# Optimization experiments

Measured on AMD Instinct MI355X. Metric: run time of the kernel, lower is better.

Reference implementation:

```python
import jax, jax.numpy as jnp
import numpy as np

B, L, H, V, G, TGB = 128, 512, 256, 100000, 4, 128
S = 2 * L - 1  # max_sequence_tokens = 2*history_capacity - 1


def setup_inputs() -> dict:
    key = jax.random.key(0)
    ks = jax.random.split(key, 16)
    d = {}
    d['history_tokens'] = jax.random.randint(ks[0], (B, L), 0, V)
    d['history_post_tokens'] = jax.random.randint(ks[1], (B, L), 0, V)
    d['history_author_tokens'] = jax.random.randint(ks[2], (B, L), 0, V)
    d['history_action_tokens'] = jax.random.randint(ks[3], (B, L), 0, V)
    d['history_time_gap'] = jax.random.randint(ks[4], (B, L), 0, TGB + 1)
    d['history_group_ids'] = jnp.sort(jax.random.randint(ks[5], (B, L), 0, G + 1), axis=-1)
    d['lengths'] = jax.random.randint(ks[6], (B,), 0, L + 1)
    # embedding tables (padding_idx=0 rows zeroed as in nn.Embedding(padding_idx=0))
    d['token_table'] = (jax.random.normal(ks[7], (V, H)) * 0.02).at[0].set(0.0)
    d['time_table'] = (jax.random.normal(ks[8], (TGB + 1, H)) * 0.02).at[0].set(0.0)
    d['group_table'] = (jax.random.normal(ks[9], (G + 1, H)) * 0.02).at[0].set(0.0)
    d['pos_table'] = jax.random.normal(ks[10], (S, H)) * 0.02
    d['sep_token'] = jax.random.normal(ks[11], (H,)) * 0.02
    # event_projection params: LayerNorm(6H) -> Linear(6H,4H) -> SiLU -> Linear(4H,H)
    d['ln_gamma'] = jnp.ones((6 * H,), jnp.float32)
    d['ln_beta'] = jnp.zeros((6 * H,), jnp.float32)
    d['W1'] = jax.random.normal(ks[12], (6 * H, 4 * H)) * (1.0 / np.sqrt(6 * H))
    d['b1'] = jnp.zeros((4 * H,), jnp.float32)
    d['W2'] = jax.random.normal(ks[13], (4 * H, H)) * (1.0 / np.sqrt(4 * H))
    d['b2'] = jnp.zeros((H,), jnp.float32)
    return d


def _layernorm(x, g, b, eps=1e-5):
    m = x.mean(-1, keepdims=True)
    v = x.var(-1, keepdims=True)
    return (x - m) / jnp.sqrt(v + eps) * g + b


def reference(history_tokens, history_post_tokens, history_author_tokens,
              history_action_tokens, history_time_gap, history_group_ids,
              lengths, token_table, time_table, group_table, pos_table,
              sep_token, ln_gamma, ln_beta, W1, b1, W2, b2):
    # --- event embedding: 6 lookups concat -> LN -> MLP  (dropout is eval no-op)
    ev = jnp.concatenate([
        token_table[history_tokens],
        token_table[history_post_tokens],
        token_table[history_author_tokens],
        token_table[history_action_tokens],
        time_table[jnp.clip(history_time_gap, 0, TGB)],
        group_table[history_group_ids],
    ], axis=-1)  # [B, L, 6H]
    h = _layernorm(ev, ln_gamma, ln_beta)
    h = jax.nn.silu(h @ W1 + b1)
    event = h @ W2 + b2  # [B, L, H]

    # --- vectorized merge_with_sep (ragged right-aligned pack with sep at group boundaries)
    pos = jnp.arange(L)
    mask = pos[None, :] < lengths[:, None]                       # prefix validity mask
    gid_next = jnp.concatenate([history_group_ids[:, 1:], history_group_ids[:, -1:]], axis=1)
    boundary = (pos[None, :] < lengths[:, None] - 1) & (history_group_ids != gid_next)
    ex = jnp.cumsum(boundary, axis=1) - boundary                 # seps strictly before event p
    event_idx = pos[None, :] + ex                                # piece index of event p
    M = lengths + boundary.sum(axis=1)                           # total pieces per row
    shift = S - M                                                # may be negative (left-truncate)
    pos_e = shift[:, None] + event_idx
    pos_s = pos_e + 1
    valid_e = mask & (pos_e >= 0)
    valid_s = boundary & (pos_s >= 0)
    barange = jnp.arange(B)[:, None]
    buf = jnp.zeros((B, S + 1, H), event.dtype)                  # extra slot S = trash bin
    buf = buf.at[barange, jnp.where(valid_e, pos_e, S)].set(
        jnp.where(valid_e[..., None], event, 0.0))
    buf = buf.at[barange, jnp.where(valid_s, pos_s, S)].set(
        jnp.where(valid_s[..., None], sep_token, 0.0))
    merged = buf[:, :S]
    merged_mask = jnp.arange(S)[None, :] >= jnp.maximum(shift, 0)[:, None]
    merged = (merged + pos_table[None]) * merged_mask[..., None].astype(merged.dtype)
    return merged, merged_mask
```

## Files before the change

### kernel.cpp

```cpp
#include <hip/hip_runtime.h>

#define B_    128
#define L_    512
#define H_    256
#define TGB_  128
#define S_    1023
#define BL_   (B_ * L_)
#define SIXH  1536
#define FOURH 1024

typedef __bf16 bf16_t;
typedef bf16_t bf16x8 __attribute__((ext_vector_type(8)));
typedef float  f32x4  __attribute__((ext_vector_type(4)));
typedef unsigned short u16x4 __attribute__((ext_vector_type(4)));

template<int P> struct IC { static constexpr int v = P; };

__device__ __forceinline__ unsigned short f2bf(float f) {
    union { float f; unsigned u; } v; v.f = f;
    unsigned u = v.u;
    unsigned r = u + 0x7FFFu + ((u >> 16) & 1u);
    return (unsigned short)(r >> 16);
}

__device__ __forceinline__ void gload_lds16(const void* g, void* l) {
    __builtin_amdgcn_global_load_lds(
        (__attribute__((address_space(1))) void*)(void*)(g),
        (__attribute__((address_space(3))) void*)(l), 16, 0, 0);
}

__global__ __launch_bounds__(256) void transpose_bf16_kernel(
    const float* __restrict__ in, unsigned short* __restrict__ out,
    int R, int C)
{
    __shared__ float tile[32][33];
    int rb = blockIdx.x * 32, cb = blockIdx.y * 32;
    int tx = threadIdx.x & 31, ty = threadIdx.x >> 5;
    #pragma unroll
    for (int d = 0; d < 32; d += 8)
        tile[ty + d][tx] = in[(size_t)(rb + ty + d) * C + cb + tx];
    __syncthreads();
    #pragma unroll
    for (int d = 0; d < 32; d += 8)
        out[(size_t)(cb + ty + d) * R + rb + tx] = f2bf(tile[tx][ty + d]);
}

__global__ __launch_bounds__(256) void embed_ln_kernel(
    const int* __restrict__ tok,  const int* __restrict__ ptok,
    const int* __restrict__ atok, const int* __restrict__ actok,
    const int* __restrict__ tgap, const int* __restrict__ gid,
    const float* __restrict__ ttab, const float* __restrict__ titab,
    const float* __restrict__ gtab, const float* __restrict__ gamma,
    const float* __restrict__ beta, const int* __restrict__ row_id,
    const int* __restrict__ Vdev, unsigned short* __restrict__ xln)
{
    int j = blockIdx.x * 4 + (threadIdx.x >> 6);
    if (j >= *Vdev) return;
    int l = threadIdx.x & 63;
    int rid = row_id[j];
    int i0 = tok[rid], i1 = ptok[rid], i2 = atok[rid], i3 = actok[rid];
    int i4 = tgap[rid]; i4 = i4 < 0 ? 0 : (i4 > TGB_ ? TGB_ : i4);
    int i5 = gid[rid];
    f32x4 v[6];
    v[0] = *(const f32x4*)(ttab  + (size_t)i0 * H_ + l * 4);
    v[1] = *(const f32x4*)(ttab  + (size_t)i1 * H_ + l * 4);
    v[2] = *(const f32x4*)(ttab  + (size_t)i2 * H_ + l * 4);
    v[3] = *(const f32x4*)(ttab  + (size_t)i3 * H_ + l * 4);
    v[4] = *(const f32x4*)(titab + (size_t)i4 * H_ + l * 4);
    v[5] = *(const f32x4*)(gtab  + (size_t)i5 * H_ + l * 4);
    float s = 0.0f, sq = 0.0f;
    #pragma unroll
    for (int k = 0; k < 6; ++k)
        #pragma unroll
        for (int c = 0; c < 4; ++c) { float f = v[k][c]; s += f; sq += f * f; }
    #pragma unroll
    for (int off = 32; off > 0; off >>= 1) {
        s  += __shfl_xor(s,  off);
        sq += __shfl_xor(sq, off);
    }
    float mean = s * (1.0f / 1536.0f);
    float var  = sq * (1.0f / 1536.0f) - mean * mean;
    float rstd = rsqrtf(var + 1e-5f);
    unsigned short* orow = xln + (size_t)j * SIXH;
    #pragma unroll
    for (int k = 0; k < 6; ++k) {
        f32x4 g = *(const f32x4*)(gamma + k * H_ + l * 4);
        f32x4 b = *(const f32x4*)(beta  + k * H_ + l * 4);
        u16x4 o;
        #pragma unroll
        for (int c = 0; c < 4; ++c)
            o[c] = f2bf((v[k][c] - mean) * rstd * g[c] + b[c]);
        *(u16x4*)(orow + k * H_ + l * 4) = o;
    }
}

template<int N, int K, int NTN>
__global__ __launch_bounds__(512, 2) void gemm8_kernel(
    const unsigned short* __restrict__ A,
    const unsigned short* __restrict__ Bt,
    const float* __restrict__ bias,
    unsigned short* __restrict__ C,
    const int* __restrict__ Vdev,
    const int* __restrict__ idx_map,
    const int* __restrict__ shiftb,
    const float* __restrict__ ptab,
    const float* __restrict__ sep,
    float* __restrict__ outF)
{
    constexpr int NT = K / 64;
    constexpr int ASLOT = 256 * 64;
    constexpr int BSLOT = 128 * 64;
    extern __shared__ __align__(16) unsigned short lds[];
    unsigned short* sA = lds;
    unsigned short* sB = lds + 3 * ASLOT;

    const int V = *Vdev;
    const int nact = ((V + 255) >> 8) * NTN;
    const int bid = blockIdx.x;
    int t = threadIdx.x;

    if (bid >= nact) {
        const int nf = (int)gridDim.x - nact;
        const int w8 = t >> 6;
        const int hh = (t & 63) * 4;
        for (int u = (bid - nact) * 8 + w8; u < B_ * S_; u += nf * 8) {
            int b = u / S_;
            int s = u - b * S_;
            int shift = shiftb[b];
            float* orow = outF + ((size_t)b * S_ + s) * H_;
            if (s < shift) {
                *(f32x4*)(orow + hh) = (f32x4)0.0f;
            } else {
                int idx = idx_map[b * S_ + s];
                if (idx == -2) {
                    f32x4 pv = *(const f32x4*)(ptab + (size_t)s * H_ + hh);
                    f32x4 sv = *(const f32x4*)(sep + hh);
                    *(f32x4*)(orow + hh) = pv + sv;
                }
            }
            if ((t & 63) == 0)
                outF[(size_t)B_ * S_ * H_ + (size_t)b * S_ + s] = (s >= shift) ? 1.0f : 0.0f;
        }
        return;
    }

    const int qd = nact >> 3, rd = nact & 7, x = bid & 7, o = bid >> 3;
    const int wid = (x < rd ? x * (qd + 1) : rd * (qd + 1) + (x - rd) * qd) + o;
    const int m0 = (wid / NTN) * 256;
    const int n0 = (wid % NTN) * 128;

    int w = t >> 6, l = t & 63;
    int srow = t >> 3;
    int scg  = (t & 7) ^ (srow & 7);
    const unsigned short* Ag = A  + (size_t)(m0 + srow) * K + scg * 8;
    const unsigned short* Bg = Bt + (size_t)(n0 + srow) * K + scg * 8;
    unsigned short* stA = sA + w * 512;
    unsigned short* stB = sB + w * 512;

    int r16 = l & 15, q = l >> 4;
    int wm = w >> 1, wn = w & 1;
    int xr = r16 & 7;
    const int aoff = (wm * 64 + r16) * 64;
    const int boff = (wn * 64 + r16) * 64;
    const int c0 = ((0 + q) ^ xr) * 8;
    const int c1 = ((4 + q) ^ xr) * 8;

    f32x4 acc[4][4];
    #pragma unroll
    for (int i = 0; i < 4; ++i)
        #pragma unroll
        for (int j = 0; j < 4; ++j) acc[i][j] = (f32x4)0.0f;

    #pragma unroll
    for (int j = 0; j < 4; ++j) gload_lds16(Ag + (size_t)j * 64 * K, stA + j * 4096);
    #pragma unroll
    for (int j = 0; j < 2; ++j) gload_lds16(Bg + (size_t)j * 64 * K, stB + j * 4096);
    #pragma unroll
    for (int j = 0; j < 4; ++j) gload_lds16(Ag + (size_t)j * 64 * K + 64, stA + ASLOT + j * 4096);
    #pragma unroll
    for (int j = 0; j < 2; ++j) gload_lds16(Bg + (size_t)j * 64 * K + 64, stB + BSLOT + j * 4096);
    asm volatile("s_waitcnt vmcnt(6)\ns_barrier" ::: "memory");

    int s = 0;
    for (int kt = 0; kt < NT; ++kt) {
        const unsigned short* sAs = sA + s * ASLOT;
        const unsigned short* sBs = sB + s * BSLOT;
        int spf = s + 2; if (spf >= 3) spf -= 3;
        const size_t gofs = (size_t)(kt + 2) * 64;
        unsigned short* pA = stA + spf * ASLOT;
        unsigned short* pB = stB + spf * BSLOT;

        bf16x8 af[4][2];
        #pragma unroll
        for (int mi = 0; mi < 4; ++mi) {
            af[mi][0] = *(const bf16x8*)(sAs + aoff + mi * 1024 + c0);
            af[mi][1] = *(const bf16x8*)(sAs + aoff + mi * 1024 + c1);
        }
        #pragma unroll
        for (int ni = 0; ni < 4; ++ni) {
            bf16x8 b0 = *(const bf16x8*)(sBs + boff + ni * 1024 + c0);
            bf16x8 b1 = *(const bf16x8*)(sBs + boff + ni * 1024 + c1);
            if (kt + 2 < NT) {
                if (ni == 0) {
                    gload_lds16(Ag + gofs,                    pA);
                    gload_lds16(Ag + (size_t) 64 * K + gofs,  pA + 4096);
                } else if (ni == 1) {
                    gload_lds16(Ag + (size_t)128 * K + gofs,  pA + 8192);
                    gload_lds16(Ag + (size_t)192 * K + gofs,  pA + 12288);
                } else if (ni == 2) {
                    gload_lds16(Bg + gofs,                    pB);
                } else {
                    gload_lds16(Bg + (size_t) 64 * K + gofs,  pB + 4096);
                }
            }
            __builtin_amdgcn_s_setprio(1);
            #pragma unroll
            for (int mi = 0; mi < 4; ++mi) {
                acc[mi][ni] = __builtin_amdgcn_mfma_f32_16x16x32_bf16(af[mi][0], b0, acc[mi][ni], 0, 0, 0);
                acc[mi][ni] = __builtin_amdgcn_mfma_f32_16x16x32_bf16(af[mi][1], b1, acc[mi][ni], 0, 0, 0);
            }
            __builtin_amdgcn_s_setprio(0);
        }
        if (kt + 2 < NT)      asm volatile("s_waitcnt vmcnt(6)\ns_barrier" ::: "memory");
        else if (kt + 1 < NT) asm volatile("s_waitcnt vmcnt(0)\ns_barrier" ::: "memory");
        s = (s == 2) ? 0 : s + 1;
    }

    #pragma unroll
    for (int mi = 0; mi < 4; ++mi) {
        #pragma unroll
        for (int ni = 0; ni < 4; ++ni) {
            int col = n0 + wn * 64 + ni * 16 + r16;
            float bv = bias[col];
            #pragma unroll
            for (int j = 0; j < 4; ++j) {
                int row = m0 + wm * 64 + mi * 16 + q * 4 + j;
                float v = acc[mi][ni][j] + bv;
                v = v / (1.0f + __expf(-v));
                C[(size_t)row * N + col] = f2bf(v);
            }
        }
    }
}

template<int K, int NTN>
__global__ __launch_bounds__(256, 2) void gemm128s_kernel(
    const unsigned short* __restrict__ A,
    const unsigned short* __restrict__ Bt,
    const float* __restrict__ bias,
    const int* __restrict__ outslot,
    const int* __restrict__ posC,
    const float* __restrict__ ptab,
    float* __restrict__ outF,
    const int* __restrict__ Vdev)
{
    constexpr int NT = K / 64;
    constexpr int IT = NT / 2;
    extern __shared__ __align__(16) unsigned short lds[];

    const int V = *Vdev;
    const int nact = ((V + 127) >> 7) * NTN;
    const int q = nact >> 3, r = nact & 7;

    const int t = threadIdx.x;
    const int w = t >> 6, l = t & 63;
    const int wm = w >> 1, wn = w & 1;
    const int r16 = l & 15, ql = l >> 4;
    const int sg = (t & 3) ^ ((t >> 3) & 3);
    unsigned short* ldsb = lds + w * 512;
    const int fr = (ql ^ ((r16 >> 1) & 3)) * 8;

    const unsigned short* la0 = lds + (wm * 64 + r16) * 32 + fr;
    const unsigned short* la1 = la0 + 16384;
    const unsigned short* lb0 = lds + 8192 + (wn * 64 + r16) * 32 + fr;
    const unsigned short* lb1 = lb0 + 16384;

    for (int bidv = blockIdx.x; bidv < nact; bidv += (int)gridDim.x) {
        const int x = bidv & 7, o = bidv >> 3;
        const int wid = (x < r ? x * (q + 1) : r * (q + 1) + (x - r) * q) + o;
        const int mt  = wid / NTN;
        const int m0  = mt * 128;
        const int n0  = (wid - mt * NTN) * 128;

        const unsigned short* As0 = A  + (size_t)(m0 + (t >> 2)) * K + sg * 8;
        const unsigned short* As1 = As0 + (size_t)64 * K;
        const unsigned short* Bs0 = Bt + (size_t)(n0 + (t >> 2)) * K + sg * 8;
        const unsigned short* Bs1 = Bs0 + (size_t)64 * K;

        f32x4 acc[4][4];
        #pragma unroll
        for (int i = 0; i < 4; ++i)
            #pragma unroll
            for (int j = 0; j < 4; ++j) acc[i][j] = (f32x4)0.0f;

        auto ST2 = [&](const unsigned short* s0, const unsigned short* s1,
                       int dofs, int gofs) {
            gload_lds16(s0 + gofs, ldsb + dofs);
            gload_lds16(s1 + gofs, ldsb + dofs + 2048);
        };

        if (bidv != (int)blockIdx.x) __syncthreads();

        ST2(As0, As1, 0,     0);
        ST2(Bs0, Bs1, 8192,  0);
        ST2(As0, As1, 4096,  32);
        ST2(Bs0, Bs1, 12288, 32);
        ST2(As0, As1, 16384, 64);
        ST2(Bs0, Bs1, 24576, 64);
        asm volatile("s_waitcnt vmcnt(4)\ns_barrier" ::: "memory");

        bf16x8 bq[4];

        auto phase = [&](auto pc, bool last) {
            constexpr int P   = decltype(pc)::v;
            constexpr int BUF = P >> 2;
            constexpr int KK  = (P & 3) >> 1;
            constexpr int MH  = P & 1;
            const unsigned short* ab = (BUF ? la1 : la0) + KK * 4096 + MH * 1024;
            bf16x8 aq[2];
            if constexpr (MH == 0) {
                const unsigned short* bb = (BUF ? lb1 : lb0) + KK * 4096;
                bq[0] = *(const bf16x8*)(bb);
                bq[1] = *(const bf16x8*)(bb + 512);
                bq[2] = *(const bf16x8*)(bb + 1024);
                bq[3] = *(const bf16x8*)(bb + 1536);
            }
            aq[0] = *(const bf16x8*)(ab);
            aq[1] = *(const bf16x8*)(ab + 512);
            if constexpr (P == 0)      {            ST2(As0, As1, 20480, 96);  }
            else if constexpr (P == 1) {            ST2(Bs0, Bs1, 28672, 96);  }
            else if constexpr (P == 2) { if (!last) ST2(As0, As1, 0,     128); }
            else if constexpr (P == 3) { if (!last) ST2(Bs0, Bs1, 8192,  128); }
            else if constexpr (P == 4) { if (!last) ST2(As0, As1, 4096,  160); }
            else if constexpr (P == 5) { if (!last) ST2(Bs0, Bs1, 12288, 160); }
            else if constexpr (P == 6) { if (!last) ST2(As0, As1, 16384, 192); }
            else                       { if (!last) ST2(Bs0, Bs1, 24576, 192); }
            asm volatile("s_barrier" ::: "memory");
            __builtin_amdgcn_s_setprio(1);
            #pragma unroll
            for (int mm = 0; mm < 2; ++mm)
                #pragma unroll
                for (int nn = 0; nn < 4; ++nn)
                    acc[MH * 2 + mm][nn] = __builtin_amdgcn_mfma_f32_16x16x32_bf16(
                        aq[mm], bq[nn], acc[MH * 2 + mm][nn], 0, 0, 0);
            __builtin_amdgcn_s_setprio(0);
            if constexpr (P == 3) {
                if (last) asm volatile("s_waitcnt vmcnt(0)\ns_barrier" ::: "memory");
                else      asm volatile("s_waitcnt vmcnt(4)\ns_barrier" ::: "memory");
            } else if constexpr (P == 7) {
                if (!last) asm volatile("s_waitcnt vmcnt(4)\ns_barrier" ::: "memory");
            } else {
                asm volatile("s_barrier" ::: "memory");
            }
        };

        for (int it = 0; it < IT; ++it) {
            const bool last = (it == IT - 1);
            phase(IC<0>{}, last);
            phase(IC<1>{}, last);
            phase(IC<2>{}, last);
            phase(IC<3>{}, last);
            phase(IC<4>{}, last);
            phase(IC<5>{}, last);
            phase(IC<6>{}, last);
            phase(IC<7>{}, last);
            As0 += 128; As1 += 128; Bs0 += 128; Bs1 += 128;
        }

        #pragma unroll
        for (int mi = 0; mi < 4; ++mi) {
            #pragma unroll
            for (int j = 0; j < 4; ++j) {
                int row = m0 + wm * 64 + mi * 16 + ql * 4 + j;
                int slot = outslot[row];
                if (slot >= 0) {
                    float* orow = outF + (size_t)slot * H_;
                    const float* prow = ptab + (size_t)posC[row] * H_;
                    #pragma unroll
                    for (int ni = 0; ni < 4; ++ni) {
                        int col = n0 + wn * 64 + ni * 16 + r16;
                        orow[col] = acc[mi][ni][j] + bias[col] + prow[col];
                    }
                }
            }
        }
    }
}

__global__ __launch_bounds__(512) void scan_scatter_kernel(
    const int* __restrict__ gid, const int* __restrict__ lengths,
    int* __restrict__ idx_map, int* __restrict__ shiftb,
    int* __restrict__ row_id, int* __restrict__ outslot,
    int* __restrict__ posC, int* __restrict__ Vdev)
{
    int b = blockIdx.x, i = threadIdx.x;
    __shared__ int slen[128];
    __shared__ int sres[2];
    if (i < 128) slen[i] = lengths[i];
    __syncthreads();
    if (i < 64) {
        int vpart = (i < b ? slen[i] : 0) + (i + 64 < b ? slen[i + 64] : 0);
        int vall  = slen[i] + slen[i + 64];
        #pragma unroll
        for (int off = 32; off > 0; off >>= 1) {
            vpart += __shfl_xor(vpart, off);
            vall  += __shfl_xor(vall,  off);
        }
        if (i == 0) { sres[0] = vpart; sres[1] = vall; }
    }
    int len = lengths[b];
    int g  = gid[b * L_ + i];
    int gn = (i < L_ - 1) ? gid[b * L_ + i + 1] : g;
    int bnd = (i < len - 1 && g != gn) ? 1 : 0;
    __shared__ int sc[512];
    sc[i] = bnd;
    __syncthreads();
    for (int off = 1; off < 512; off <<= 1) {
        int v = (i >= off) ? sc[i - off] : 0;
        __syncthreads();
        sc[i] += v;
        __syncthreads();
    }
    int incl  = sc[i];
    int total = sc[511];
    int ex = incl - bnd;
    int M = len + total;
    int shift = S_ - M;
    int pb = sres[0], V = sres[1];
    for (int s = i; s < S_; s += 512) idx_map[b * S_ + s] = -1;
    __syncthreads();
    if (i < len) {
        int p = shift + i + ex;
        idx_map[b * S_ + p] = i;
        if (bnd) idx_map[b * S_ + p + 1] = -2;
        int j = pb + i;
        row_id[j]  = b * L_ + i;
        outslot[j] = b * S_ + p;
        posC[j]    = p;
    }
    if (i == 0) shiftb[b] = shift;
    if (b == B_ - 1) {
        if (i == 0) *Vdev = V;
        if (i < 256) outslot[V + i] = -1;
    }
}

extern "C" void kernel_launch(void* const* d_in, const int* in_sizes, int n_in,
                              void* d_out, int out_size, void* d_ws, size_t ws_size,
                              hipStream_t stream)
{
    const int*   tok   = (const int*)d_in[0];
    const int*   ptok  = (const int*)d_in[1];
    const int*   atok  = (const int*)d_in[2];
    const int*   actok = (const int*)d_in[3];
    const int*   tgap  = (const int*)d_in[4];
    const int*   gid   = (const int*)d_in[5];
    const int*   lens  = (const int*)d_in[6];
    const float* ttab  = (const float*)d_in[7];
    const float* titab = (const float*)d_in[8];
    const float* gtab  = (const float*)d_in[9];
    const float* post  = (const float*)d_in[10];
    const float* sep   = (const float*)d_in[11];
    const float* gamma = (const float*)d_in[12];
    const float* beta  = (const float*)d_in[13];
    const float* W1    = (const float*)d_in[14];
    const float* b1    = (const float*)d_in[15];
    const float* W2    = (const float*)d_in[16];
    const float* b2    = (const float*)d_in[17];

    unsigned short* xln  = (unsigned short*)d_ws;
    unsigned short* hbuf = xln  + (size_t)BL_ * SIXH;
    unsigned short* W1T  = hbuf + (size_t)BL_ * FOURH;
    unsigned short* W2T  = W1T  + (size_t)FOURH * SIXH;
    int* idx_map = (int*)(W2T + (size_t)H_ * FOURH);
    int* shiftb  = idx_map + B_ * S_;
    int* Vdev    = shiftb + B_;
    int* row_id  = Vdev + 4;
    int* outslot = row_id + BL_;
    int* posC    = outslot + BL_ + 256;
    float* out   = (float*)d_out;

    constexpr int LDS1 = 3 * (256 * 64 + 128 * 64) * 2;
    constexpr int LDS2 = 2 * 16384 * 2;
    (void)hipFuncSetAttribute((const void*)&gemm8_kernel<FOURH, SIXH, 8>,
                              hipFuncAttributeMaxDynamicSharedMemorySize, LDS1);
    (void)hipFuncSetAttribute((const void*)&gemm128s_kernel<FOURH, 2>,
                              hipFuncAttributeMaxDynamicSharedMemorySize, LDS2);

    transpose_bf16_kernel<<<dim3(SIXH / 32, FOURH / 32), 256, 0, stream>>>(W1, W1T, SIXH, FOURH);
    transpose_bf16_kernel<<<dim3(FOURH / 32, H_ / 32),   256, 0, stream>>>(W2, W2T, FOURH, H_);

    scan_scatter_kernel<<<B_, 512, 0, stream>>>(gid, lens, idx_map, shiftb,
                                                row_id, outslot, posC, Vdev);

    embed_ln_kernel<<<BL_ / 4, 256, 0, stream>>>(tok, ptok, atok, actok, tgap, gid,
                                                 ttab, titab, gtab, gamma, beta,
                                                 row_id, Vdev, xln);

    gemm8_kernel<FOURH, SIXH, 8><<<2560, 512, LDS1, stream>>>(
        xln, W1T, b1, hbuf, Vdev, idx_map, shiftb, post, sep, out);
    gemm128s_kernel<FOURH, 2><<<1024, 256, LDS2, stream>>>(
        hbuf, W2T, b2, outslot, posC, post, out, Vdev);
}
```

Baseline: 266.7 us.

## Merge weight transpose, scan and embed-LN into one preprocessing kernel

Replaces four launches (two weight transposes, the scan/scatter, and the embedding+LayerNorm) with a single block-partitioned kernel. Embedding blocks now compute their compacted row index themselves from a prefix sum over lengths, rather than reading a row_id array written by the scan kernel. This removes the dependency between those stages and the row_id buffer. The stages can then run concurrently and launch overheads drop. In exchange, every embedding warp redoes a small prefix reduction, and blocks for padded events exit early.

```diff
diff --git a/kernel.cpp b/kernel.cpp
--- a/kernel.cpp
+++ b/kernel.cpp
@@ -29,68 +29,145 @@
         (__attribute__((address_space(3))) void*)(l), 16, 0, 0);
 }
 
-__global__ __launch_bounds__(256) void transpose_bf16_kernel(
-    const float* __restrict__ in, unsigned short* __restrict__ out,
-    int R, int C)
-{
-    __shared__ float tile[32][33];
-    int rb = blockIdx.x * 32, cb = blockIdx.y * 32;
-    int tx = threadIdx.x & 31, ty = threadIdx.x >> 5;
-    #pragma unroll
-    for (int d = 0; d < 32; d += 8)
-        tile[ty + d][tx] = in[(size_t)(rb + ty + d) * C + cb + tx];
-    __syncthreads();
-    #pragma unroll
-    for (int d = 0; d < 32; d += 8)
-        out[(size_t)(cb + ty + d) * R + rb + tx] = f2bf(tile[tx][ty + d]);
-}
-
-__global__ __launch_bounds__(256) void embed_ln_kernel(
+__global__ __launch_bounds__(512) void pre_kernel(
     const int* __restrict__ tok,  const int* __restrict__ ptok,
     const int* __restrict__ atok, const int* __restrict__ actok,
     const int* __restrict__ tgap, const int* __restrict__ gid,
+    const int* __restrict__ lengths,
     const float* __restrict__ ttab, const float* __restrict__ titab,
     const float* __restrict__ gtab, const float* __restrict__ gamma,
-    const float* __restrict__ beta, const int* __restrict__ row_id,
-    const int* __restrict__ Vdev, unsigned short* __restrict__ xln)
+    const float* __restrict__ beta,
+    const float* __restrict__ W1, const float* __restrict__ W2,
+    unsigned short* __restrict__ W1T, unsigned short* __restrict__ W2T,
+    unsigned short* __restrict__ xln,
+    int* __restrict__ idx_map, int* __restrict__ shiftb,
+    int* __restrict__ outslot, int* __restrict__ posC,
+    int* __restrict__ Vdev)
 {
-    int j = blockIdx.x * 4 + (threadIdx.x >> 6);
-    if (j >= *Vdev) return;
-    int l = threadIdx.x & 63;
-    int rid = row_id[j];
-    int i0 = tok[rid], i1 = ptok[rid], i2 = atok[rid], i3 = actok[rid];
-    int i4 = tgap[rid]; i4 = i4 < 0 ? 0 : (i4 > TGB_ ? TGB_ : i4);
-    int i5 = gid[rid];
-    f32x4 v[6];
-    v[0] = *(const f32x4*)(ttab  + (size_t)i0 * H_ + l * 4);
-    v[1] = *(const f32x4*)(ttab  + (size_t)i1 * H_ + l * 4);
-    v[2] = *(const f32x4*)(ttab  + (size_t)i2 * H_ + l * 4);
-    v[3] = *(const f32x4*)(ttab  + (size_t)i3 * H_ + l * 4);
-    v[4] = *(const f32x4*)(titab + (size_t)i4 * H_ + l * 4);
-    v[5] = *(const f32x4*)(gtab  + (size_t)i5 * H_ + l * 4);
-    float s = 0.0f, sq = 0.0f;
-    #pragma unroll
-    for (int k = 0; k < 6; ++k)
-        #pragma unroll
-        for (int c = 0; c < 4; ++c) { float f = v[k][c]; s += f; sq += f * f; }
-    #pragma unroll
-    for (int off = 32; off > 0; off >>= 1) {
-        s  += __shfl_xor(s,  off);
-        sq += __shfl_xor(sq, off);
-    }
-    float mean = s * (1.0f / 1536.0f);
-    float var  = sq * (1.0f / 1536.0f) - mean * mean;
-    float rstd = rsqrtf(var + 1e-5f);
-    unsigned short* orow = xln + (size_t)j * SIXH;
-    #pragma unroll
-    for (int k = 0; k < 6; ++k) {
-        f32x4 g = *(const f32x4*)(gamma + k * H_ + l * 4);
-        f32x4 b = *(const f32x4*)(beta  + k * H_ + l * 4);
-        u16x4 o;
-        #pragma unroll
-        for (int c = 0; c < 4; ++c)
-            o[c] = f2bf((v[k][c] - mean) * rstd * g[c] + b[c]);
-        *(u16x4*)(orow + k * H_ + l * 4) = o;
+    int blk = blockIdx.x, i = threadIdx.x;
+
+    if (blk >= 1024) {
+        int eblk = blk - 1024;
+        int b = eblk >> 6;
+        int w = i >> 6, l = i & 63;
+        int ei = (eblk & 63) * 8 + w;
+        int len = lengths[b];
+        if (ei >= len) return;
+        int vpart = (l < b ? lengths[l] : 0) + (l + 64 < b ? lengths[l + 64] : 0);
+        #pragma unroll
+        for (int off = 32; off > 0; off >>= 1) vpart += __shfl_xor(vpart, off);
+        int j = vpart + ei;
+        int rid = b * L_ + ei;
+        int i0 = tok[rid], i1 = ptok[rid], i2 = atok[rid], i3 = actok[rid];
+        int i4 = tgap[rid]; i4 = i4 < 0 ? 0 : (i4 > TGB_ ? TGB_ : i4);
+        int i5 = gid[rid];
+        f32x4 v[6];
+        v[0] = *(const f32x4*)(ttab  + (size_t)i0 * H_ + l * 4);
+        v[1] = *(const f32x4*)(ttab  + (size_t)i1 * H_ + l * 4);
+        v[2] = *(const f32x4*)(ttab  + (size_t)i2 * H_ + l * 4);
+        v[3] = *(const f32x4*)(ttab  + (size_t)i3 * H_ + l * 4);
+        v[4] = *(const f32x4*)(titab + (size_t)i4 * H_ + l * 4);
+        v[5] = *(const f32x4*)(gtab  + (size_t)i5 * H_ + l * 4);
+        float s = 0.0f, sq = 0.0f;
+        #pragma unroll
+        for (int k = 0; k < 6; ++k)
+            #pragma unroll
+            for (int c = 0; c < 4; ++c) { float f = v[k][c]; s += f; sq += f * f; }
+        #pragma unroll
+        for (int off = 32; off > 0; off >>= 1) {
+            s  += __shfl_xor(s,  off);
+            sq += __shfl_xor(sq, off);
+        }
+        float mean = s * (1.0f / 1536.0f);
+        float var  = sq * (1.0f / 1536.0f) - mean * mean;
+        float rstd = rsqrtf(var + 1e-5f);
+        unsigned short* orow = xln + (size_t)j * SIXH;
+        #pragma unroll
+        for (int k = 0; k < 6; ++k) {
+            f32x4 g = *(const f32x4*)(gamma + k * H_ + l * 4);
+            f32x4 bb = *(const f32x4*)(beta + k * H_ + l * 4);
+            u16x4 o;
+            #pragma unroll
+            for (int c = 0; c < 4; ++c)
+                o[c] = f2bf((v[k][c] - mean) * rstd * g[c] + bb[c]);
+            *(u16x4*)(orow + k * H_ + l * 4) = o;
+        }
+        return;
+    }
+
+    if (blk >= B_) {
+        __shared__ float tile[2][32][33];
+        int half = i >> 8;
+        int t = i & 255;
+        int tidx = (blk - B_) * 2 + half;
+        const float* in; unsigned short* out; int R, C, rb, cb;
+        if (tidx < 1536) {
+            in = W1; out = W1T; R = SIXH; C = FOURH;
+            rb = (tidx % 48) * 32; cb = (tidx / 48) * 32;
+        } else {
+            int u = tidx - 1536;
+            in = W2; out = W2T; R = FOURH; C = H_;
+            rb = (u % 32) * 32; cb = (u / 32) * 32;
+        }
+        int tx = t & 31, ty = t >> 5;
+        #pragma unroll
+        for (int d = 0; d < 32; d += 8)
+            tile[half][ty + d][tx] = in[(size_t)(rb + ty + d) * C + cb + tx];
+        __syncthreads();
+        #pragma unroll
+        for (int d = 0; d < 32; d += 8)
+            out[(size_t)(cb + ty + d) * R + rb + tx] = f2bf(tile[half][tx][ty + d]);
+        return;
+    }
+
+    int b = blk;
+    __shared__ int slen[128];
+    __shared__ int sres[2];
+    if (i < 128) slen[i] = lengths[i];
+    __syncthreads();
+    if (i < 64) {
+        int vpart = (i < b ? slen[i] : 0) + (i + 64 < b ? slen[i + 64] : 0);
+        int vall  = slen[i] + slen[i + 64];
+        #pragma unroll
+        for (int off = 32; off > 0; off >>= 1) {
+            vpart += __shfl_xor(vpart, off);
+            vall  += __shfl_xor(vall,  off);
+        }
+        if (i == 0) { sres[0] = vpart; sres[1] = vall; }
+    }
+    int len = lengths[b];
+    int g  = gid[b * L_ + i];
+    int gn = (i < L_ - 1) ? gid[b * L_ + i + 1] : g;
+    int bnd = (i < len - 1 && g != gn) ? 1 : 0;
+    __shared__ int sc[512];
+    sc[i] = bnd;
+    __syncthreads();
+    for (int off = 1; off < 512; off <<= 1) {
+        int v = (i >= off) ? sc[i - off] : 0;
+        __syncthreads();
+        sc[i] += v;
+        __syncthreads();
+    }
+    int incl  = sc[i];
+    int total = sc[511];
+    int ex = incl - bnd;
+    int M = len + total;
+    int shift = S_ - M;
+    int pb = sres[0], V = sres[1];
+    for (int s = i; s < S_; s += 512) idx_map[b * S_ + s] = -1;
+    __syncthreads();
+    if (i < len) {
+        int p = shift + i + ex;
+        idx_map[b * S_ + p] = i;
+        if (bnd) idx_map[b * S_ + p + 1] = -2;
+        int j = pb + i;
+        outslot[j] = b * S_ + p;
+        posC[j]    = p;
+    }
+    if (i == 0) shiftb[b] = shift;
+    if (b == B_ - 1) {
+        if (i == 0) *Vdev = V;
+        if (i < 256) outslot[V + i] = -1;
     }
 }
 
@@ -384,64 +461,6 @@
                 }
             }
         }
-    }
-}
-
-__global__ __launch_bounds__(512) void scan_scatter_kernel(
-    const int* __restrict__ gid, const int* __restrict__ lengths,
-    int* __restrict__ idx_map, int* __restrict__ shiftb,
-    int* __restrict__ row_id, int* __restrict__ outslot,
-    int* __restrict__ posC, int* __restrict__ Vdev)
-{
-    int b = blockIdx.x, i = threadIdx.x;
-    __shared__ int slen[128];
-    __shared__ int sres[2];
-    if (i < 128) slen[i] = lengths[i];
-    __syncthreads();
-    if (i < 64) {
-        int vpart = (i < b ? slen[i] : 0) + (i + 64 < b ? slen[i + 64] : 0);
-        int vall  = slen[i] + slen[i + 64];
-        #pragma unroll
-        for (int off = 32; off > 0; off >>= 1) {
-            vpart += __shfl_xor(vpart, off);
-            vall  += __shfl_xor(vall,  off);
-        }
-        if (i == 0) { sres[0] = vpart; sres[1] = vall; }
-    }
-    int len = lengths[b];
-    int g  = gid[b * L_ + i];
-    int gn = (i < L_ - 1) ? gid[b * L_ + i + 1] : g;
-    int bnd = (i < len - 1 && g != gn) ? 1 : 0;
-    __shared__ int sc[512];
-    sc[i] = bnd;
-    __syncthreads();
-    for (int off = 1; off < 512; off <<= 1) {
-        int v = (i >= off) ? sc[i - off] : 0;
-        __syncthreads();
-        sc[i] += v;
-        __syncthreads();
-    }
-    int incl  = sc[i];
-    int total = sc[511];
-    int ex = incl - bnd;
-    int M = len + total;
-    int shift = S_ - M;
-    int pb = sres[0], V = sres[1];
-    for (int s = i; s < S_; s += 512) idx_map[b * S_ + s] = -1;
-    __syncthreads();
-    if (i < len) {
-        int p = shift + i + ex;
-        idx_map[b * S_ + p] = i;
-        if (bnd) idx_map[b * S_ + p + 1] = -2;
-        int j = pb + i;
-        row_id[j]  = b * L_ + i;
-        outslot[j] = b * S_ + p;
-        posC[j]    = p;
-    }
-    if (i == 0) shiftb[b] = shift;
-    if (b == B_ - 1) {
-        if (i == 0) *Vdev = V;
-        if (i < 256) outslot[V + i] = -1;
     }
 }
 
@@ -475,8 +494,7 @@
     int* idx_map = (int*)(W2T + (size_t)H_ * FOURH);
     int* shiftb  = idx_map + B_ * S_;
     int* Vdev    = shiftb + B_;
-    int* row_id  = Vdev + 4;
-    int* outslot = row_id + BL_;
+    int* outslot = Vdev + 4;
     int* posC    = outslot + BL_ + 256;
     float* out   = (float*)d_out;
 
@@ -487,15 +505,11 @@
     (void)hipFuncSetAttribute((const void*)&gemm128s_kernel<FOURH, 2>,
                               hipFuncAttributeMaxDynamicSharedMemorySize, LDS2);
 
-    transpose_bf16_kernel<<<dim3(SIXH / 32, FOURH / 32), 256, 0, stream>>>(W1, W1T, SIXH, FOURH);
-    transpose_bf16_kernel<<<dim3(FOURH / 32, H_ / 32),   256, 0, stream>>>(W2, W2T, FOURH, H_);
-
-    scan_scatter_kernel<<<B_, 512, 0, stream>>>(gid, lens, idx_map, shiftb,
-                                                row_id, outslot, posC, Vdev);
-
-    embed_ln_kernel<<<BL_ / 4, 256, 0, stream>>>(tok, ptok, atok, actok, tgap, gid,
-                                                 ttab, titab, gtab, gamma, beta,
-                                                 row_id, Vdev, xln);
+    pre_kernel<<<1024 + BL_ / 8, 512, 0, stream>>>(
+        tok, ptok, atok, actok, tgap, gid, lens,
+        ttab, titab, gtab, gamma, beta,
+        W1, W2, W1T, W2T, xln,
+        idx_map, shiftb, outslot, posC, Vdev);
 
     gemm8_kernel<FOURH, SIXH, 8><<<2560, 512, LDS1, stream>>>(
         xln, W1T, b1, hbuf, Vdev, idx_map, shiftb, post, sep, out);
```

Measured after the change: 271.2 us. About the same (+1.7%).
